# Kernel optimization log

Hardware: AMD Instinct MI355X
Metric: run time of the kernel (lower is better)

Reference implementation:

```python
import jax, jax.numpy as jnp
import numpy as np

N_NODES = 50000
N_HYPEREDGES = 50000
E = 320000
D = 256


def _prelu(x, a):
    return jnp.where(x >= 0, x, a * x)


def _hypergraph_conv(x, hei, W, b, num_nodes, num_edges):
    # PyG HypergraphConv, use_attention=False, heads=1:
    # out = D^{-1} H B^{-1} H^T (X W^T) + b
    src = hei[0]  # node indices, [E]
    he = hei[1]   # hyperedge indices, [E]
    xw = x @ W.T  # [N, D] node transform (lin has no bias)
    ones = jnp.ones((hei.shape[1],), x.dtype)
    deg_n = jax.ops.segment_sum(ones, src, num_segments=num_nodes)   # node degree D
    deg_e = jax.ops.segment_sum(ones, he, num_segments=num_edges)    # hyperedge size B
    d_inv = jnp.where(deg_n > 0, 1.0 / deg_n, 0.0)
    b_inv = jnp.where(deg_e > 0, 1.0 / deg_e, 0.0)
    # node -> hyperedge aggregation, scaled by B^{-1}
    edge_feat = b_inv[:, None] * jax.ops.segment_sum(xw[src], he, num_segments=num_edges)  # [n_he, D]
    # hyperedge -> node aggregation, scaled by D^{-1}
    out = d_inv[:, None] * jax.ops.segment_sum(edge_feat[he], src, num_segments=num_nodes)  # [N, D]
    return out + b


def setup_inputs() -> dict:
    key = jax.random.key(0)
    ks = jax.random.split(key, 6)
    std = np.sqrt(2.0 / D)  # kaiming_normal
    x = jax.random.normal(ks[0], (N_NODES, D), dtype=jnp.float32)
    hyper_edge_index = jax.random.randint(ks[1], (2, E), 0, N_HYPEREDGES, dtype=jnp.int64)
    W1 = jax.random.normal(ks[2], (D, D), dtype=jnp.float32) * std
    b1 = jnp.zeros((D,), jnp.float32)
    W2 = jax.random.normal(ks[3], (D, D), dtype=jnp.float32) * std
    b2 = jnp.zeros((D,), jnp.float32)
    prelu_a = jnp.asarray(0.25, jnp.float32)
    return {"x": x, "W1": W1, "b1": b1, "W2": W2, "b2": b2,
            "prelu_a": prelu_a, "hyper_edge_index": hyper_edge_index}


def reference(x, W1, b1, W2, b2, prelu_a, hyper_edge_index):
    out = _hypergraph_conv(x, hyper_edge_index, W1, b1, N_NODES, N_HYPEREDGES)
    out = _prelu(out, prelu_a)
    out = _hypergraph_conv(out, hyper_edge_index, W2, b2, N_NODES, N_HYPEREDGES)
    out = out + x  # residual
    out = _prelu(out, prelu_a)
    return out
```

## Files before the change

### kernel.cpp

```cpp
#include <hip/hip_runtime.h>

#define NN    50000
#define NHE   50000
#define NEDGE 320000
#define DD    256

#define SB    1024
#define NBLK  ((NN + SB - 1) / SB)
#define CNTB  ((NEDGE / 4 + 255) / 256)

typedef float f32x4 __attribute__((ext_vector_type(4)));
typedef short short8 __attribute__((ext_vector_type(8)));

static __device__ __forceinline__ unsigned short f2b(float f) {
    union { float f; unsigned u; } c; c.f = f;
    unsigned u = c.u;
    u += 0x7fffu + ((u >> 16) & 1u);
    return (unsigned short)(u >> 16);
}
static __device__ __forceinline__ float b2f_lo(unsigned v) {
    union { unsigned u; float f; } c; c.u = v << 16; return c.f;
}
static __device__ __forceinline__ float b2f_hi(unsigned v) {
    union { unsigned u; float f; } c; c.u = v & 0xffff0000u; return c.f;
}
static __device__ __forceinline__ unsigned pack2(float a, float b) {
    return (unsigned)f2b(a) | ((unsigned)f2b(b) << 16);
}

__global__ __launch_bounds__(256) void k_count_cvt(const int* __restrict__ src,
                                                   const int* __restrict__ he,
                                                   int* __restrict__ cnt_n,
                                                   int* __restrict__ cnt_e,
                                                   int* __restrict__ rank_n,
                                                   int* __restrict__ rank_e,
                                                   const float* __restrict__ w1,
                                                   const float* __restrict__ w2,
                                                   unsigned short* __restrict__ o1,
                                                   unsigned short* __restrict__ o2) {
    int bx = blockIdx.x;
    if (bx >= CNTB) {
        int t = (bx - CNTB) * 256 + threadIdx.x;
        const int n4 = DD * DD / 4;
        const float* s = (t < n4) ? w1 : w2;
        unsigned short* d = (t < n4) ? o1 : o2;
        int i = (t < n4) ? t : t - n4;
        float4 v = ((const float4*)s)[i];
        uint2 o;
        o.x = pack2(v.x, v.y);
        o.y = pack2(v.z, v.w);
        ((uint2*)d)[i] = o;
        return;
    }
    int t  = bx * 256 + threadIdx.x;
    int e0 = t * 4;
    if (e0 >= NEDGE) return;
    int4 s = *(const int4*)(src + e0);
    int4 h = *(const int4*)(he + e0);
    int4 rn, re;
    rn.x = atomicAdd(&cnt_n[s.x], 1);
    rn.y = atomicAdd(&cnt_n[s.y], 1);
    rn.z = atomicAdd(&cnt_n[s.z], 1);
    rn.w = atomicAdd(&cnt_n[s.w], 1);
    re.x = atomicAdd(&cnt_e[h.x], 1);
    re.y = atomicAdd(&cnt_e[h.y], 1);
    re.z = atomicAdd(&cnt_e[h.z], 1);
    re.w = atomicAdd(&cnt_e[h.w], 1);
    *(int4*)(rank_n + e0) = rn;
    *(int4*)(rank_e + e0) = re;
}

__global__ __launch_bounds__(256) void k_scan_a(const int* __restrict__ cnt_n,
                                                const int* __restrict__ cnt_e,
                                                int* __restrict__ bsum) {
    int b   = blockIdx.x;
    int seg = b / NBLK, lb = b % NBLK;
    const int* cnt = seg ? cnt_e : cnt_n;
    int t = threadIdx.x;
    int idx = lb * SB + t * 4;
    int s = 0;
#pragma unroll
    for (int j = 0; j < 4; ++j)
        if (idx + j < NN) s += cnt[idx + j];
    __shared__ int red[256];
    red[t] = s;
    __syncthreads();
    for (int o = 128; o > 0; o >>= 1) {
        if (t < o) red[t] += red[t + o];
        __syncthreads();
    }
    if (t == 0) bsum[b] = red[0];
}

__global__ __launch_bounds__(256) void k_scan_c(const int* __restrict__ cnt_n,
                                                const int* __restrict__ cnt_e,
                                                const int* __restrict__ bsum,
                                                int* __restrict__ off_n,
                                                int* __restrict__ off_e) {
    int b   = blockIdx.x;
    int seg = b / NBLK, lb = b % NBLK;
    const int* cnt = seg ? cnt_e : cnt_n;
    int* off = seg ? off_e : off_n;
    int t = threadIdx.x;
    __shared__ int sb[NBLK];
    __shared__ int binfo[2];
    if (t < NBLK) sb[t] = bsum[seg * NBLK + t];
    __syncthreads();
    if (t == 0) {
        int base = 0, tot = 0;
        for (int j = 0; j < NBLK; ++j) { if (j < lb) base += sb[j]; tot += sb[j]; }
        binfo[0] = base; binfo[1] = tot;
    }
    int idx = lb * SB + t * 4;
    int v[4];
    int tsum = 0;
#pragma unroll
    for (int j = 0; j < 4; ++j) {
        v[j] = (idx + j < NN) ? cnt[idx + j] : 0;
        tsum += v[j];
    }
    __shared__ int sc[256];
    sc[t] = tsum;
    __syncthreads();
    for (int o = 1; o < 256; o <<= 1) {
        int val = (t >= o) ? sc[t - o] : 0;
        __syncthreads();
        sc[t] += val;
        __syncthreads();
    }
    int p = binfo[0] + sc[t] - tsum;
#pragma unroll
    for (int j = 0; j < 4; ++j) {
        if (idx + j < NN) off[idx + j] = p;
        p += v[j];
    }
    if (b == 0 && t == 0) off_n[NN] = binfo[1];
    if (b == NBLK && t == 0) off_e[NHE] = binfo[1];
}

__global__ __launch_bounds__(256) void k_fill(const int* __restrict__ src,
                                              const int* __restrict__ he,
                                              const int* __restrict__ off_n,
                                              const int* __restrict__ off_e,
                                              const int* __restrict__ rank_n,
                                              const int* __restrict__ rank_e,
                                              int* __restrict__ adj_n,
                                              int* __restrict__ adj_e) {
    int t  = blockIdx.x * 256 + threadIdx.x;
    int e0 = t * 4;
    if (e0 >= NEDGE) return;
    int4 s  = *(const int4*)(src + e0);
    int4 h  = *(const int4*)(he + e0);
    int4 rn = *(const int4*)(rank_n + e0);
    int4 re = *(const int4*)(rank_e + e0);
    int on0 = off_n[s.x], on1 = off_n[s.y], on2 = off_n[s.z], on3 = off_n[s.w];
    int oe0 = off_e[h.x], oe1 = off_e[h.y], oe2 = off_e[h.z], oe3 = off_e[h.w];
    adj_n[on0 + rn.x] = h.x;
    adj_n[on1 + rn.y] = h.y;
    adj_n[on2 + rn.z] = h.z;
    adj_n[on3 + rn.w] = h.w;
    adj_e[oe0 + re.x] = s.x;
    adj_e[oe1 + re.y] = s.y;
    adj_e[oe2 + re.z] = s.z;
    adj_e[oe3 + re.w] = s.w;
}

template <bool A32>
static __device__ __forceinline__ void gemm_direct(const void* __restrict__ Av,
                                                   const unsigned short* __restrict__ Wb,
                                                   unsigned short* __restrict__ Cb,
                                                   int M, int m0) {
    const int t    = threadIdx.x;
    const int lane = t & 63;
    const int wave = t >> 6;
    const int wm   = (wave >> 1) * 32;
    const int wn   = (wave & 1) * 128;
    const int fr   = lane & 15;
    const int fq   = lane >> 4;

    f32x4 acc[2][8] = {};

    int arow0 = m0 + wm + fr;      if (arow0 >= M) arow0 = M - 1;
    int arow1 = m0 + wm + 16 + fr; if (arow1 >= M) arow1 = M - 1;

#pragma unroll
    for (int k0 = 0; k0 < DD; k0 += 32) {
        short8 af[2], bf[8];
        if (A32) {
            const float* p0 = (const float*)Av + (size_t)arow0 * DD + k0 + fq * 8;
            const float* p1 = (const float*)Av + (size_t)arow1 * DD + k0 + fq * 8;
            float4 a0 = ((const float4*)p0)[0];
            float4 a1 = ((const float4*)p0)[1];
            float4 a2 = ((const float4*)p1)[0];
            float4 a3 = ((const float4*)p1)[1];
            uint4 u0, u1;
            u0.x = pack2(a0.x, a0.y); u0.y = pack2(a0.z, a0.w);
            u0.z = pack2(a1.x, a1.y); u0.w = pack2(a1.z, a1.w);
            u1.x = pack2(a2.x, a2.y); u1.y = pack2(a2.z, a2.w);
            u1.z = pack2(a3.x, a3.y); u1.w = pack2(a3.z, a3.w);
            af[0] = *(short8*)&u0;
            af[1] = *(short8*)&u1;
        } else {
            af[0] = *(const short8*)((const unsigned short*)Av + (size_t)arow0 * DD + k0 + fq * 8);
            af[1] = *(const short8*)((const unsigned short*)Av + (size_t)arow1 * DD + k0 + fq * 8);
        }
#pragma unroll
        for (int nt = 0; nt < 8; ++nt)
            bf[nt] = *(const short8*)(Wb + (size_t)(wn + nt * 16 + fr) * DD + k0 + fq * 8);
#pragma unroll
        for (int mt = 0; mt < 2; ++mt)
#pragma unroll
            for (int nt = 0; nt < 8; ++nt)
                acc[mt][nt] = __builtin_amdgcn_mfma_f32_16x16x32_bf16(af[mt], bf[nt],
                                                                      acc[mt][nt], 0, 0, 0);
    }

#pragma unroll
    for (int mt = 0; mt < 2; ++mt)
#pragma unroll
        for (int i = 0; i < 4; ++i) {
            int gm = m0 + wm + mt * 16 + fq * 4 + i;
            if (gm >= M) continue;
#pragma unroll
            for (int nt = 0; nt < 8; ++nt)
                Cb[(size_t)gm * DD + wn + nt * 16 + fr] = f2b(acc[mt][nt][i]);
        }
}

__global__ __launch_bounds__(256) void k_gemm1(const float* __restrict__ x,
                                               const unsigned short* __restrict__ Wb,
                                               unsigned short* __restrict__ Cb) {
    gemm_direct<true>((const void*)x, Wb, Cb, NN, blockIdx.x * 64);
}
__global__ __launch_bounds__(256) void k_gemm2(const unsigned short* __restrict__ Av,
                                               const unsigned short* __restrict__ Wb,
                                               unsigned short* __restrict__ Cb) {
    gemm_direct<false>((const void*)Av, Wb, Cb, NN, blockIdx.x * 64);
}

static __device__ __forceinline__ void acc8(float* a, uint4 v) {
    a[0] += b2f_lo(v.x); a[1] += b2f_hi(v.x);
    a[2] += b2f_lo(v.y); a[3] += b2f_hi(v.y);
    a[4] += b2f_lo(v.z); a[5] += b2f_hi(v.z);
    a[6] += b2f_lo(v.w); a[7] += b2f_hi(v.w);
}
static __device__ __forceinline__ void gather8(const unsigned short* __restrict__ srcb,
                                               const int* __restrict__ adj,
                                               int b, int e, int sl, float* a) {
#pragma unroll
    for (int i = 0; i < 8; ++i) a[i] = 0.f;
    for (int i = b; i < e; i += 8) {
        int g0 = adj[i];
        int g[8];
        g[0] = g0;
#pragma unroll
        for (int j = 1; j < 8; ++j) g[j] = (i + j < e) ? adj[i + j] : g0;
        uint4 v[8];
#pragma unroll
        for (int j = 0; j < 8; ++j)
            v[j] = *(const uint4*)(srcb + (size_t)g[j] * DD + sl * 8);
        acc8(a, v[0]);
#pragma unroll
        for (int j = 1; j < 8; ++j)
            if (i + j < e) acc8(a, v[j]);
    }
}

__global__ __launch_bounds__(256) void k_gather_edge_b(const unsigned short* __restrict__ xw,
                                                       unsigned short* __restrict__ ef,
                                                       const int* __restrict__ off,
                                                       const int* __restrict__ adj) {
    int tid = blockIdx.x * 256 + threadIdx.x;
    int w = tid >> 5;
    int sl = tid & 31;
    if (w >= NHE) return;
    int b = off[w], e = off[w + 1];
    float a[8];
    gather8(xw, adj, b, e, sl, a);
    float sc = (e > b) ? 1.f / (float)(e - b) : 0.f;
    uint4 o;
    o.x = pack2(a[0] * sc, a[1] * sc);
    o.y = pack2(a[2] * sc, a[3] * sc);
    o.z = pack2(a[4] * sc, a[5] * sc);
    o.w = pack2(a[6] * sc, a[7] * sc);
    *(uint4*)(ef + (size_t)w * DD + sl * 8) = o;
}

__global__ __launch_bounds__(256) void k_gather_node_mid_b(const unsigned short* __restrict__ ef,
                                                           unsigned short* __restrict__ h,
                                                           const int* __restrict__ off,
                                                           const int* __restrict__ adj,
                                                           const float* __restrict__ bias,
                                                           const float* __restrict__ aP) {
    int tid = blockIdx.x * 256 + threadIdx.x;
    int w = tid >> 5;
    int sl = tid & 31;
    if (w >= NN) return;
    int b = off[w], e = off[w + 1];
    float a[8];
    gather8(ef, adj, b, e, sl, a);
    float sc = (e > b) ? 1.f / (float)(e - b) : 0.f;
    float al = *aP;
    float4 bb0 = ((const float4*)bias)[sl * 2];
    float4 bb1 = ((const float4*)bias)[sl * 2 + 1];
    float r[8];
    r[0] = a[0] * sc + bb0.x; r[1] = a[1] * sc + bb0.y;
    r[2] = a[2] * sc + bb0.z; r[3] = a[3] * sc + bb0.w;
    r[4] = a[4] * sc + bb1.x; r[5] = a[5] * sc + bb1.y;
    r[6] = a[6] * sc + bb1.z; r[7] = a[7] * sc + bb1.w;
#pragma unroll
    for (int i = 0; i < 8; ++i) r[i] = (r[i] >= 0.f) ? r[i] : al * r[i];
    uint4 o;
    o.x = pack2(r[0], r[1]);
    o.y = pack2(r[2], r[3]);
    o.z = pack2(r[4], r[5]);
    o.w = pack2(r[6], r[7]);
    *(uint4*)(h + (size_t)w * DD + sl * 8) = o;
}

__global__ __launch_bounds__(256) void k_gather_node_final_b(const unsigned short* __restrict__ ef,
                                                             const float* __restrict__ x,
                                                             float* __restrict__ out,
                                                             const int* __restrict__ off,
                                                             const int* __restrict__ adj,
                                                             const float* __restrict__ bias,
                                                             const float* __restrict__ aP) {
    int tid = blockIdx.x * 256 + threadIdx.x;
    int w = tid >> 5;
    int sl = tid & 31;
    if (w >= NN) return;
    int b = off[w], e = off[w + 1];
    float a[8];
    gather8(ef, adj, b, e, sl, a);
    float sc = (e > b) ? 1.f / (float)(e - b) : 0.f;
    float al = *aP;
    float4 bb0 = ((const float4*)bias)[sl * 2];
    float4 bb1 = ((const float4*)bias)[sl * 2 + 1];
    const float* xp = x + (size_t)w * DD + sl * 8;
    float4 xv0 = *(const float4*)xp;
    float4 xv1 = *(const float4*)(xp + 4);
    float r[8];
    r[0] = a[0] * sc + bb0.x + xv0.x; r[1] = a[1] * sc + bb0.y + xv0.y;
    r[2] = a[2] * sc + bb0.z + xv0.z; r[3] = a[3] * sc + bb0.w + xv0.w;
    r[4] = a[4] * sc + bb1.x + xv1.x; r[5] = a[5] * sc + bb1.y + xv1.y;
    r[6] = a[6] * sc + bb1.z + xv1.z; r[7] = a[7] * sc + bb1.w + xv1.w;
#pragma unroll
    for (int i = 0; i < 8; ++i) r[i] = (r[i] >= 0.f) ? r[i] : al * r[i];
    float* op = out + (size_t)w * DD + sl * 8;
    *(float4*)op = make_float4(r[0], r[1], r[2], r[3]);
    *(float4*)(op + 4) = make_float4(r[4], r[5], r[6], r[7]);
}

extern "C" void kernel_launch(void* const* d_in, const int* in_sizes, int n_in,
                              void* d_out, int out_size, void* d_ws, size_t ws_size,
                              hipStream_t stream) {
    const float* x       = (const float*)d_in[0];
    const float* W1      = (const float*)d_in[1];
    const float* b1      = (const float*)d_in[2];
    const float* W2      = (const float*)d_in[3];
    const float* b2      = (const float*)d_in[4];
    const float* prelu_a = (const float*)d_in[5];
    const int*   hei     = (const int*)d_in[6];
    const int* idx_src = hei;
    const int* idx_he  = hei + NEDGE;

    float* out = (float*)d_out;
    unsigned short* B1 = (unsigned short*)d_ws;
    unsigned short* B2 = B1 + (size_t)NN * DD;
    int* off_n  = (int*)(B2 + (size_t)NN * DD);
    int* off_e  = off_n + NN + 1;
    int* cnt_n  = off_e + NHE + 1;
    int* cnt_e  = cnt_n + NN;
    int* adj_n  = cnt_e + NHE;
    int* adj_e  = adj_n + NEDGE;
    int* rank_n = adj_e + NEDGE;
    int* rank_e = rank_n + NEDGE;
    int* bsum   = rank_e + NEDGE;
    unsigned short* w1b = (unsigned short*)d_out;
    unsigned short* w2b = w1b + DD * DD;

    const int gblocks = (NN * 32 + 255) / 256;
    const int mblocks = (NN + 63) / 64;

    hipMemsetAsync(cnt_n, 0, sizeof(int) * (NN + NHE), stream);
    k_count_cvt<<<CNTB + 128, 256, 0, stream>>>(idx_src, idx_he, cnt_n, cnt_e,
                                                rank_n, rank_e, W1, W2, w1b, w2b);
    k_scan_a<<<2 * NBLK, 256, 0, stream>>>(cnt_n, cnt_e, bsum);
    k_scan_c<<<2 * NBLK, 256, 0, stream>>>(cnt_n, cnt_e, bsum, off_n, off_e);
    k_fill<<<CNTB, 256, 0, stream>>>(idx_src, idx_he, off_n, off_e,
                                     rank_n, rank_e, adj_n, adj_e);

    k_gemm1<<<mblocks, 256, 0, stream>>>(x, w1b, B1);
    k_gather_edge_b<<<gblocks, 256, 0, stream>>>(B1, B2, off_e, adj_e);
    k_gather_node_mid_b<<<gblocks, 256, 0, stream>>>(B2, B1, off_n, adj_n, b1, prelu_a);

    k_gemm2<<<mblocks, 256, 0, stream>>>(B1, w2b, B2);
    k_gather_edge_b<<<gblocks, 256, 0, stream>>>(B2, B1, off_e, adj_e);
    k_gather_node_final_b<<<gblocks, 256, 0, stream>>>(B1, x, out, off_n, adj_n, b2, prelu_a);
}
```

Measured before the change: 351.2 us.

## Stage half of bf16 weight in swizzled LDS and stream A rows per wave

New measurement: 310.5 us. 11.6% less time.

```diff
diff --git a/kernel.cpp b/kernel.cpp
--- a/kernel.cpp
+++ b/kernel.cpp
@@ -26,6 +26,12 @@
 }
 static __device__ __forceinline__ unsigned pack2(float a, float b) {
     return (unsigned)f2b(a) | ((unsigned)f2b(b) << 16);
+}
+
+static __device__ __forceinline__ void glds16(const unsigned short* g, unsigned short* l) {
+    __builtin_amdgcn_global_load_lds((const __attribute__((address_space(1))) unsigned int*)g,
+                                     (__attribute__((address_space(3))) unsigned int*)l,
+                                     16, 0, 0);
 }
 
 __global__ __launch_bounds__(256) void k_count_cvt(const int* __restrict__ src,
@@ -166,76 +172,67 @@
 }
 
 template <bool A32>
-static __device__ __forceinline__ void gemm_direct(const void* __restrict__ Av,
-                                                   const unsigned short* __restrict__ Wb,
-                                                   unsigned short* __restrict__ Cb,
-                                                   int M, int m0) {
+__global__ __launch_bounds__(1024) void k_gemm_bres(const void* __restrict__ Av,
+                                                    const unsigned short* __restrict__ Wb,
+                                                    unsigned short* __restrict__ Cb) {
+    __shared__ __align__(16) unsigned short Bs[128 * 256];
     const int t    = threadIdx.x;
     const int lane = t & 63;
     const int wave = t >> 6;
-    const int wm   = (wave >> 1) * 32;
-    const int wn   = (wave & 1) * 128;
-    const int fr   = lane & 15;
-    const int fq   = lane >> 4;
-
-    f32x4 acc[2][8] = {};
-
-    int arow0 = m0 + wm + fr;      if (arow0 >= M) arow0 = M - 1;
-    int arow1 = m0 + wm + 16 + fr; if (arow1 >= M) arow1 = M - 1;
-
-#pragma unroll
-    for (int k0 = 0; k0 < DD; k0 += 32) {
-        short8 af[2], bf[8];
-        if (A32) {
-            const float* p0 = (const float*)Av + (size_t)arow0 * DD + k0 + fq * 8;
-            const float* p1 = (const float*)Av + (size_t)arow1 * DD + k0 + fq * 8;
-            float4 a0 = ((const float4*)p0)[0];
-            float4 a1 = ((const float4*)p0)[1];
-            float4 a2 = ((const float4*)p1)[0];
-            float4 a3 = ((const float4*)p1)[1];
-            uint4 u0, u1;
-            u0.x = pack2(a0.x, a0.y); u0.y = pack2(a0.z, a0.w);
-            u0.z = pack2(a1.x, a1.y); u0.w = pack2(a1.z, a1.w);
-            u1.x = pack2(a2.x, a2.y); u1.y = pack2(a2.z, a2.w);
-            u1.z = pack2(a3.x, a3.y); u1.w = pack2(a3.z, a3.w);
-            af[0] = *(short8*)&u0;
-            af[1] = *(short8*)&u1;
-        } else {
-            af[0] = *(const short8*)((const unsigned short*)Av + (size_t)arow0 * DD + k0 + fq * 8);
-            af[1] = *(const short8*)((const unsigned short*)Av + (size_t)arow1 * DD + k0 + fq * 8);
+    const int n0   = blockIdx.x * 128;
+
+#pragma unroll
+    for (int q = 0; q < 4; ++q) {
+        int row   = q * 32 + wave * 2 + (lane >> 5);
+        int chunk = lane & 31;
+        glds16(Wb + (size_t)(n0 + row) * DD + ((chunk ^ (row & 7)) * 8),
+               Bs + q * 8192 + wave * 512);
+    }
+    __syncthreads();
+
+    const int fr = lane & 15;
+    const int fq = lane >> 4;
+    int chunk = blockIdx.y * 16 + wave;
+    if (chunk * 16 >= NN) return;
+    int m0 = chunk * 16;
+
+    f32x4 acc[8] = {};
+    short8 af[8];
+    if (A32) {
+        const float* p = (const float*)Av + (size_t)(m0 + fr) * DD + fq * 8;
+#pragma unroll
+        for (int kc = 0; kc < 8; ++kc) {
+            const float* pp = p + kc * 32;
+            float4 f0 = ((const float4*)pp)[0];
+            float4 f1 = ((const float4*)pp)[1];
+            uint4 u;
+            u.x = pack2(f0.x, f0.y); u.y = pack2(f0.z, f0.w);
+            u.z = pack2(f1.x, f1.y); u.w = pack2(f1.z, f1.w);
+            af[kc] = *(short8*)&u;
         }
-#pragma unroll
-        for (int nt = 0; nt < 8; ++nt)
-            bf[nt] = *(const short8*)(Wb + (size_t)(wn + nt * 16 + fr) * DD + k0 + fq * 8);
-#pragma unroll
-        for (int mt = 0; mt < 2; ++mt)
-#pragma unroll
-            for (int nt = 0; nt < 8; ++nt)
-                acc[mt][nt] = __builtin_amdgcn_mfma_f32_16x16x32_bf16(af[mt], bf[nt],
-                                                                      acc[mt][nt], 0, 0, 0);
-    }
-
-#pragma unroll
-    for (int mt = 0; mt < 2; ++mt)
-#pragma unroll
-        for (int i = 0; i < 4; ++i) {
-            int gm = m0 + wm + mt * 16 + fq * 4 + i;
-            if (gm >= M) continue;
-#pragma unroll
-            for (int nt = 0; nt < 8; ++nt)
-                Cb[(size_t)gm * DD + wn + nt * 16 + fr] = f2b(acc[mt][nt][i]);
+    } else {
+        const unsigned short* p = (const unsigned short*)Av + (size_t)(m0 + fr) * DD + fq * 8;
+#pragma unroll
+        for (int kc = 0; kc < 8; ++kc)
+            af[kc] = *(const short8*)(p + kc * 32);
+    }
+
+#pragma unroll
+    for (int kc = 0; kc < 8; ++kc) {
+#pragma unroll
+        for (int nt = 0; nt < 8; ++nt) {
+            int r  = nt * 16 + fr;
+            int ch = (kc * 4 + fq) ^ (fr & 7);
+            short8 bf = *(const short8*)(Bs + r * 256 + ch * 8);
+            acc[nt] = __builtin_amdgcn_mfma_f32_16x16x32_bf16(af[kc], bf, acc[nt], 0, 0, 0);
         }
-}
-
-__global__ __launch_bounds__(256) void k_gemm1(const float* __restrict__ x,
-                                               const unsigned short* __restrict__ Wb,
-                                               unsigned short* __restrict__ Cb) {
-    gemm_direct<true>((const void*)x, Wb, Cb, NN, blockIdx.x * 64);
-}
-__global__ __launch_bounds__(256) void k_gemm2(const unsigned short* __restrict__ Av,
-                                               const unsigned short* __restrict__ Wb,
-                                               unsigned short* __restrict__ Cb) {
-    gemm_direct<false>((const void*)Av, Wb, Cb, NN, blockIdx.x * 64);
+    }
+
+#pragma unroll
+    for (int nt = 0; nt < 8; ++nt)
+#pragma unroll
+        for (int i = 0; i < 4; ++i)
+            Cb[(size_t)(m0 + fq * 4 + i) * DD + n0 + nt * 16 + fr] = f2b(acc[nt][i]);
 }
 
 static __device__ __forceinline__ void acc8(float* a, uint4 v) {
@@ -380,7 +377,7 @@
     unsigned short* w2b = w1b + DD * DD;
 
     const int gblocks = (NN * 32 + 255) / 256;
-    const int mblocks = (NN + 63) / 64;
+    dim3 ggrid(2, (NN / 16 + 15) / 16);
 
     hipMemsetAsync(cnt_n, 0, sizeof(int) * (NN + NHE), stream);
     k_count_cvt<<<CNTB + 128, 256, 0, stream>>>(idx_src, idx_he, cnt_n, cnt_e,
@@ -390,11 +387,11 @@
     k_fill<<<CNTB, 256, 0, stream>>>(idx_src, idx_he, off_n, off_e,
                                      rank_n, rank_e, adj_n, adj_e);
 
-    k_gemm1<<<mblocks, 256, 0, stream>>>(x, w1b, B1);
+    k_gemm_bres<true><<<ggrid, 1024, 0, stream>>>((const void*)x, w1b, B1);
     k_gather_edge_b<<<gblocks, 256, 0, stream>>>(B1, B2, off_e, adj_e);
     k_gather_node_mid_b<<<gblocks, 256, 0, stream>>>(B2, B1, off_n, adj_n, b1, prelu_a);
 
-    k_gemm2<<<mblocks, 256, 0, stream>>>(B1, w2b, B2);
+    k_gemm_bres<false><<<ggrid, 1024, 0, stream>>>((const void*)B1, w2b, B2);
     k_gather_edge_b<<<gblocks, 256, 0, stream>>>(B2, B1, off_e, adj_e);
     k_gather_node_final_b<<<gblocks, 256, 0, stream>>>(B1, x, out, off_n, adj_n, b2, prelu_a);
 }
```
